# Optimization experiments

Hardware: AMD Instinct MI355X
Metric: run time of the kernel (lower is better)

Reference implementation:

```python
import jax, jax.numpy as jnp
import numpy as np

N_HEADS = 16
MAX_LEN = 1024


def setup_inputs() -> dict:
    key = jax.random.key(0)
    ks = jax.random.split(key, 6)
    B, T, C = 4, 1024, 1024
    scale = 0.02
    return {
        "x": jax.random.normal(ks[0], (B, T, C), dtype=jnp.float32),
        "qkv_w": jax.random.normal(ks[1], (3 * C, C), dtype=jnp.float32) * scale,
        "qkv_b": jax.random.normal(ks[2], (3 * C,), dtype=jnp.float32) * scale,
        "proj_w": jax.random.normal(ks[3], (C, C), dtype=jnp.float32) * scale,
        "proj_b": jax.random.normal(ks[4], (C,), dtype=jnp.float32) * scale,
        "rel_pos_emb": jax.random.normal(ks[5], (2 * MAX_LEN - 1, C), dtype=jnp.float32) * scale,
    }


def reference(x, qkv_w, qkv_b, proj_w, proj_b, rel_pos_emb):
    B, T, C = x.shape
    H = N_HEADS
    D = C // H
    # QKV projection: (B,T,3C) -> (3,B,H,T,D)
    qkv = (x @ qkv_w.T + qkv_b).reshape(B, T, 3, H, D)
    qkv = jnp.transpose(qkv, (2, 0, 3, 1, 4))
    q, k, v = qkv[0], qkv[1], qkv[2]
    # scores: (B,H,T,T)
    att = jnp.einsum("bhtd,bhsd->bhts", q, k) / np.sqrt(D).astype(np.float32)
    # Relative position bias: gather-then-sum == sum-then-gather over head_dim.
    # Pre-reduce table to (2*max_len-1, H) to avoid materializing (T,T,C).
    table = rel_pos_emb.reshape(2 * MAX_LEN - 1, H, D).sum(axis=-1)  # (2L-1, H)
    pos = jnp.arange(T)
    rel_idx = pos[:, None] - pos[None, :] + (MAX_LEN - 1)  # (T,T)
    bias = jnp.transpose(table[rel_idx], (2, 0, 1))  # (H,T,T)
    att = att + bias[None]
    # causal mask: positions j > i masked to -inf
    causal = pos[None, :] > pos[:, None]  # (T,T) True above diagonal
    att = jnp.where(causal[None, None], -jnp.inf, att)
    att = jax.nn.softmax(att, axis=-1)
    out = jnp.einsum("bhts,bhsd->bhtd", att, v)  # (B,H,T,D)
    out = jnp.transpose(out, (0, 2, 1, 3)).reshape(B, T, C)
    return out @ proj_w.T + proj_b
```

## Files before the change

### kernel.cpp

```cpp
#include <hip/hip_runtime.h>
#include <hip/hip_bf16.h>
#include <cstdint>


typedef __bf16 bf16x8 __attribute__((ext_vector_type(8)));
typedef float f32x4 __attribute__((ext_vector_type(4)));

__device__ __forceinline__ float bf2f(unsigned short u) {
    return __uint_as_float(((unsigned)u) << 16);
}
__device__ __forceinline__ unsigned short f2bf(float f) {
    __hip_bfloat16 h = __float2bfloat16(f);
    return *reinterpret_cast<unsigned short*>(&h);
}
__device__ __forceinline__ int4 cvt8(float4 a, float4 b) {
    union { unsigned short s[8]; int4 v; } u;
    u.s[0] = f2bf(a.x); u.s[1] = f2bf(a.y); u.s[2] = f2bf(a.z); u.s[3] = f2bf(a.w);
    u.s[4] = f2bf(b.x); u.s[5] = f2bf(b.y); u.s[6] = f2bf(b.z); u.s[7] = f2bf(b.w);
    return u.v;
}

__device__ __forceinline__ void gload16(const void* g, void* l) {
    __builtin_amdgcn_global_load_lds(
        reinterpret_cast<const __attribute__((address_space(1))) unsigned int*>(
            reinterpret_cast<uintptr_t>(g)),
        reinterpret_cast<__attribute__((address_space(3))) unsigned int*>(
            reinterpret_cast<uintptr_t>(l)),
        16, 0, 0);
}

__global__ __launch_bounds__(256) void cvt3(const float* __restrict__ x,
                                            const float* __restrict__ w1,
                                            const float* __restrict__ w2,
                                            unsigned short* __restrict__ ox,
                                            unsigned short* __restrict__ ow1,
                                            unsigned short* __restrict__ ow2) {
    const int i = blockIdx.x * 256 + threadIdx.x;
    const float* s; unsigned short* d; int li;
    if (i < 524288)      { s = x;  d = ox;  li = i; }
    else if (i < 917504) { s = w1; d = ow1; li = i - 524288; }
    else                 { s = w2; d = ow2; li = i - 917504; }
    const float4 a = *(const float4*)(s + (size_t)li * 8);
    const float4 b = *(const float4*)(s + (size_t)li * 8 + 4);
    *(int4*)(d + (size_t)li * 8) = cvt8(a, b);
}

__global__ __launch_bounds__(256) void table_reduce(const float* __restrict__ rel,
                                                    float* __restrict__ table) {
    const int p = blockIdx.x;
    const int tid = threadIdx.x, lane = tid & 63, wave = tid >> 6;
    const float* r = rel + (size_t)p * 1024;
    float s[4];
#pragma unroll
    for (int k = 0; k < 4; ++k) s[k] = r[tid + 256 * k];
#pragma unroll
    for (int k = 0; k < 4; ++k) {
        float v = s[k];
        for (int o = 32; o; o >>= 1) v += __shfl_xor(v, o, 64);
        if (lane == 0) table[p * 16 + wave + 4 * k] = v;
    }
}

template <int EPI>
__global__ __launch_bounds__(512) void gemm_bt(const unsigned short* __restrict__ A,
                                               const unsigned short* __restrict__ B,
                                               const float* __restrict__ bias,
                                               unsigned short* __restrict__ outb,
                                               float* __restrict__ outf,
                                               int M, int N, int K) {
    __shared__ __attribute__((aligned(16))) unsigned short As[128 * 32];
    __shared__ __attribute__((aligned(16))) unsigned short Bs[128 * 32];
    const int bm = blockIdx.x * 128, bn = blockIdx.y * 128;
    const int tid = threadIdx.x, lane = tid & 63, wave = tid >> 6;
    const int wr = wave & 1, wc = wave >> 1;
    const int quad = lane >> 4, lm = lane & 15;

    const int srow = tid >> 2;
    const int scol = (tid & 3) * 8;
    const unsigned short* Ap = A + (size_t)(bm + srow) * K + scol;
    const unsigned short* Bp = B + (size_t)(bn + srow) * K + scol;
    unsigned short* AsW = &As[tid * 8];
    unsigned short* BsW = &Bs[tid * 8];

    f32x4 acc[4][2];
#pragma unroll
    for (int r = 0; r < 4; ++r)
#pragma unroll
        for (int c = 0; c < 2; ++c) acc[r][c] = (f32x4){0.f, 0.f, 0.f, 0.f};

    for (int kk = 0; kk < K; kk += 32) {
        gload16(Ap + kk, AsW);
        gload16(Bp + kk, BsW);
        __syncthreads();

        bf16x8 af[4], bfr[2];
#pragma unroll
        for (int r = 0; r < 4; ++r)
            af[r] = *(const bf16x8*)(&As[(64 * wr + 16 * r + lm) * 32 + quad * 8]);
#pragma unroll
        for (int c = 0; c < 2; ++c)
            bfr[c] = *(const bf16x8*)(&Bs[(32 * wc + 16 * c + lm) * 32 + quad * 8]);
#pragma unroll
        for (int r = 0; r < 4; ++r)
#pragma unroll
            for (int c = 0; c < 2; ++c)
                acc[r][c] = __builtin_amdgcn_mfma_f32_16x16x32_bf16(af[r], bfr[c], acc[r][c], 0, 0, 0);
        __syncthreads();
    }

#pragma unroll
    for (int r = 0; r < 4; ++r)
#pragma unroll
        for (int c = 0; c < 2; ++c)
#pragma unroll
            for (int i = 0; i < 4; ++i) {
                const int row = bm + 64 * wr + 16 * r + quad * 4 + i;
                const int col = bn + 32 * wc + 16 * c + lm;
                const float v = acc[r][c][i] + bias[col];
                if (EPI == 0) {
                    const int b = row >> 10, t = row & 1023;
                    const int s3 = col >> 10, rem = col & 1023;
                    const int h = rem >> 6, d = rem & 63;
                    const size_t base = (((size_t)s3 * 4 + b) * 16 + h) * 65536;
                    const size_t off = base + (s3 == 2 ? (size_t)d * 1024 + t
                                                       : (size_t)t * 64 + d);
                    outb[off] = f2bf(v);
                } else {
                    outf[(size_t)row * N + col] = v;
                }
            }
}


#define LOADK(DST, KT)                                                        \
    do {                                                                      \
        _Pragma("unroll")                                                     \
        for (int nb = 0; nb < 4; ++nb) {                                      \
            const size_t kr = (size_t)((KT) * 64 + nb * 16 + lm) * 64;        \
            DST[nb * 2]     = *(const bf16x8*)(Kg + kr + quad * 8);           \
            DST[nb * 2 + 1] = *(const bf16x8*)(Kg + kr + 32 + quad * 8);      \
        }                                                                     \
    } while (0)

#define ATTN_TILE(KF, KT)                                                     \
    do {                                                                      \
        const int kt_ = (KT);                                                 \
            \
        bf16x8 vf[8];                                                         \
        _Pragma("unroll")                                                     \
        for (int nb = 0; nb < 4; ++nb) {                                      \
            const size_t vr = (size_t)(nb * 16 + lm) * 1024 + (size_t)kt_ * 64; \
            vf[nb * 2]     = *(const bf16x8*)(Vtg + vr + quad * 8);           \
            vf[nb * 2 + 1] = *(const bf16x8*)(Vtg + vr + 32 + quad * 8);      \
        }                                                                     \
                                \
        f32x4 s[4];                                                           \
        _Pragma("unroll")                                                     \
        for (int nb = 0; nb < 4; ++nb) {                                      \
            s[nb] = (f32x4){0.f, 0.f, 0.f, 0.f};                              \
            s[nb] = __builtin_amdgcn_mfma_f32_16x16x32_bf16(KF[nb * 2], qf0, s[nb], 0, 0, 0); \
            s[nb] = __builtin_amdgcn_mfma_f32_16x16x32_bf16(KF[nb * 2 + 1], qf1, s[nb], 0, 0, 0); \
        }                                                                     \
                    \
        const int jb0 = kt_ * 64 + quad * 4;                                  \
        _Pragma("unroll")                                                     \
        for (int nb = 0; nb < 4; ++nb)                                        \
            _Pragma("unroll")                                                 \
            for (int i = 0; i < 4; ++i) {                                     \
                const int j = jb0 + nb * 16 + i;                              \
                const float v = fmaf(s[nb][i], 0.125f, tb[q - j + 127]);      \
                s[nb][i] = (j <= q) ? v : -1e30f;                             \
            }                                                                 \
              \
        float mx = -1e30f;                                                    \
        _Pragma("unroll")                                                     \
        for (int nb = 0; nb < 4; ++nb)                                        \
            _Pragma("unroll")                                                 \
            for (int i = 0; i < 4; ++i) mx = fmaxf(mx, s[nb][i]);             \
        mx = fmaxf(mx, __shfl_xor(mx, 16, 64));                               \
        mx = fmaxf(mx, __shfl_xor(mx, 32, 64));                               \
        const float mnew = fmaxf(mi, mx);                                     \
        const float alpha = __expf(mi - mnew);                                \
        mi = mnew;                                                            \
        _Pragma("unroll")                                                     \
        for (int nb = 0; nb < 4; ++nb)                                        \
            _Pragma("unroll")                                                 \
            for (int i = 0; i < 4; ++i) s[nb][i] = __expf(s[nb][i] - mnew);   \
        float psum = 0.f;                                                     \
        _Pragma("unroll")                                                     \
        for (int nb = 0; nb < 4; ++nb)                                        \
            psum += (s[nb][0] + s[nb][1]) + (s[nb][2] + s[nb][3]);            \
        psum += __shfl_xor(psum, 16, 64);                                     \
        psum += __shfl_xor(psum, 32, 64);                                     \
        li = li * alpha + psum;                                               \
         \
        _Pragma("unroll")                                                     \
        for (int nb = 0; nb < 4; ++nb) {                                      \
            union { unsigned short u[4]; int2 v; } p4;                        \
            p4.u[0] = f2bf(s[nb][0]);                                         \
            p4.u[1] = f2bf(s[nb][1]);                                         \
            p4.u[2] = f2bf(s[nb][2]);                                         \
            p4.u[3] = f2bf(s[nb][3]);                                         \
            *(int2*)(&Ps[wave][lm][nb * 16 + quad * 4]) = p4.v;               \
        }                                                                     \
                        \
        _Pragma("unroll")                                                     \
        for (int nb = 0; nb < 4; ++nb)                                        \
            _Pragma("unroll")                                                 \
            for (int i = 0; i < 4; ++i) oacc[nb][i] *= alpha;                 \
        const bf16x8 p0 = *(const bf16x8*)(&Ps[wave][lm][quad * 8]);          \
        const bf16x8 p1 = *(const bf16x8*)(&Ps[wave][lm][32 + quad * 8]);     \
                           \
        _Pragma("unroll")                                                     \
        for (int nb = 0; nb < 4; ++nb) {                                      \
            oacc[nb] = __builtin_amdgcn_mfma_f32_16x16x32_bf16(vf[nb * 2], p0, oacc[nb], 0, 0, 0); \
            oacc[nb] = __builtin_amdgcn_mfma_f32_16x16x32_bf16(vf[nb * 2 + 1], p1, oacc[nb], 0, 0, 0); \
        }                                                                     \
    } while (0)

__global__ __launch_bounds__(256) void attn_mfma(const unsigned short* __restrict__ qkvb,
                                                 const float* __restrict__ table,
                                                 unsigned short* __restrict__ y) {
    const int bh = blockIdx.x, b = bh >> 4, h = bh & 15;
    const int level = 15 - blockIdx.y;
    const int tid = threadIdx.x, lane = tid & 63, wave = tid >> 6;
    const int quad = lane >> 4, lm = lane & 15;

    __shared__ __attribute__((aligned(16))) unsigned short Ps[4][16][72];
    __shared__ float tb[1152];

    const unsigned short* Qg  = qkvb + ((size_t)(b)*16 + h) * 65536;
    const unsigned short* Kg  = qkvb + ((size_t)(4 + b)*16 + h) * 65536;
    const unsigned short* Vtg = qkvb + ((size_t)(8 + b)*16 + h) * 65536;

    const int sl = 4 * level + wave;
    const int q = 16 * sl + lm;
    const int ktiles = level + 1;

    const bf16x8 qf0 = *(const bf16x8*)(Qg + (size_t)q * 64 + quad * 8);
    const bf16x8 qf1 = *(const bf16x8*)(Qg + (size_t)q * 64 + 32 + quad * 8);

    const int tbn = 64 * level + 191;
    for (int i = tid; i < tbn; i += 256) tb[i] = table[(896 + i) * 16 + h];
    __syncthreads();

    f32x4 oacc[4];
#pragma unroll
    for (int nb = 0; nb < 4; ++nb) oacc[nb] = (f32x4){0.f, 0.f, 0.f, 0.f};
    float mi = -1e30f, li = 0.f;

    bf16x8 kA[8], kB[8];
    LOADK(kA, 0);
    int kt = 0;
    for (; kt + 2 <= ktiles; kt += 2) {
        LOADK(kB, kt + 1);
        ATTN_TILE(kA, kt);
        if (kt + 2 < ktiles) LOADK(kA, kt + 2);
        ATTN_TILE(kB, kt + 1);
    }
    if (kt < ktiles) ATTN_TILE(kA, kt);

    const float linv = 1.0f / li;
#pragma unroll
    for (int nb = 0; nb < 4; ++nb) {
        union { unsigned short u[4]; int2 v; } o4;
#pragma unroll
        for (int i = 0; i < 4; ++i) o4.u[i] = f2bf(oacc[nb][i] * linv);
        *(int2*)(y + ((size_t)(b * 1024 + q)) * 1024 + h * 64 + nb * 16 + quad * 4) = o4.v;
    }
}

extern "C" void kernel_launch(void* const* d_in, const int* in_sizes, int n_in,
                              void* d_out, int out_size, void* d_ws, size_t ws_size,
                              hipStream_t stream) {
    const float* x      = (const float*)d_in[0];
    const float* qkv_w  = (const float*)d_in[1];
    const float* qkv_b  = (const float*)d_in[2];
    const float* proj_w = (const float*)d_in[3];
    const float* proj_b = (const float*)d_in[4];
    const float* rel    = (const float*)d_in[5];
    float* out = (float*)d_out;

    char* ws = (char*)d_ws;
    unsigned short* xb   = (unsigned short*)(ws + 0);
    unsigned short* qwb  = (unsigned short*)(ws + 8388608);
    unsigned short* pwb  = (unsigned short*)(ws + 14680064);
    float* table         = (float*)(ws + 16777216);
    unsigned short* qkvb = (unsigned short*)(ws + 16908288);
    unsigned short* yb   = (unsigned short*)(ws + 42074112);

    cvt3<<<4096, 256, 0, stream>>>(x, qkv_w, proj_w, xb, qwb, pwb);
    table_reduce<<<2047, 256, 0, stream>>>(rel, table);
    gemm_bt<0><<<dim3(32, 24), 512, 0, stream>>>(xb, qwb, qkv_b, qkvb, nullptr,
                                                 4096, 3072, 1024);
    attn_mfma<<<dim3(64, 16), 256, 0, stream>>>(qkvb, table, yb);
    gemm_bt<1><<<dim3(32, 8), 512, 0, stream>>>(yb, pwb, proj_b, nullptr, out,
                                                4096, 1024, 1024);
}
```

Measured before the change: 221.7 us.

## Split attention softmax state into two independent streams over alternating key tiles

The online-softmax state (running max, sum, output accumulator and P staging buffer) is duplicated so even and odd key tiles update independent chains, which removes the serial dependency between consecutive tiles and lets their MFMA and exp work interleave. The row-sum cross-lane shuffle reduction is deferred from every tile to a single final step. The two partial states are merged at the end by rescaling to a common max. This costs an extra accumulator set in registers and doubles the LDS for P, which may raise register pressure and lower occupancy.

```diff
diff --git a/kernel.cpp b/kernel.cpp
--- a/kernel.cpp
+++ b/kernel.cpp
@@ -142,10 +142,10 @@
         }                                                                     \
     } while (0)
 
-#define ATTN_TILE(KF, KT)                                                     \
+#define ATTN_TILE(KF, KT, MI, LIP, OACC, PSB)                                 \
     do {                                                                      \
         const int kt_ = (KT);                                                 \
-            \
+                     \
         bf16x8 vf[8];                                                         \
         _Pragma("unroll")                                                     \
         for (int nb = 0; nb < 4; ++nb) {                                      \
@@ -171,7 +171,7 @@
                 const float v = fmaf(s[nb][i], 0.125f, tb[q - j + 127]);      \
                 s[nb][i] = (j <= q) ? v : -1e30f;                             \
             }                                                                 \
-              \
+         \
         float mx = -1e30f;                                                    \
         _Pragma("unroll")                                                     \
         for (int nb = 0; nb < 4; ++nb)                                        \
@@ -179,21 +179,19 @@
             for (int i = 0; i < 4; ++i) mx = fmaxf(mx, s[nb][i]);             \
         mx = fmaxf(mx, __shfl_xor(mx, 16, 64));                               \
         mx = fmaxf(mx, __shfl_xor(mx, 32, 64));                               \
-        const float mnew = fmaxf(mi, mx);                                     \
-        const float alpha = __expf(mi - mnew);                                \
-        mi = mnew;                                                            \
+        const float mnew = fmaxf(MI, mx);                                     \
+        const float alpha = __expf(MI - mnew);                                \
+        MI = mnew;                                                            \
         _Pragma("unroll")                                                     \
         for (int nb = 0; nb < 4; ++nb)                                        \
             _Pragma("unroll")                                                 \
             for (int i = 0; i < 4; ++i) s[nb][i] = __expf(s[nb][i] - mnew);   \
-        float psum = 0.f;                                                     \
-        _Pragma("unroll")                                                     \
-        for (int nb = 0; nb < 4; ++nb)                                        \
-            psum += (s[nb][0] + s[nb][1]) + (s[nb][2] + s[nb][3]);            \
-        psum += __shfl_xor(psum, 16, 64);                                     \
-        psum += __shfl_xor(psum, 32, 64);                                     \
-        li = li * alpha + psum;                                               \
-         \
+        float lsum = 0.f;                                                     \
+        _Pragma("unroll")                                                     \
+        for (int nb = 0; nb < 4; ++nb)                                        \
+            lsum += (s[nb][0] + s[nb][1]) + (s[nb][2] + s[nb][3]);            \
+        LIP = LIP * alpha + lsum;             \
+          \
         _Pragma("unroll")                                                     \
         for (int nb = 0; nb < 4; ++nb) {                                      \
             union { unsigned short u[4]; int2 v; } p4;                        \
@@ -201,20 +199,20 @@
             p4.u[1] = f2bf(s[nb][1]);                                         \
             p4.u[2] = f2bf(s[nb][2]);                                         \
             p4.u[3] = f2bf(s[nb][3]);                                         \
-            *(int2*)(&Ps[wave][lm][nb * 16 + quad * 4]) = p4.v;               \
+            *(int2*)(&PSB[wave][lm][nb * 16 + quad * 4]) = p4.v;              \
         }                                                                     \
                         \
         _Pragma("unroll")                                                     \
         for (int nb = 0; nb < 4; ++nb)                                        \
             _Pragma("unroll")                                                 \
-            for (int i = 0; i < 4; ++i) oacc[nb][i] *= alpha;                 \
-        const bf16x8 p0 = *(const bf16x8*)(&Ps[wave][lm][quad * 8]);          \
-        const bf16x8 p1 = *(const bf16x8*)(&Ps[wave][lm][32 + quad * 8]);     \
+            for (int i = 0; i < 4; ++i) OACC[nb][i] *= alpha;                 \
+        const bf16x8 p0 = *(const bf16x8*)(&PSB[wave][lm][quad * 8]);         \
+        const bf16x8 p1 = *(const bf16x8*)(&PSB[wave][lm][32 + quad * 8]);    \
                            \
         _Pragma("unroll")                                                     \
         for (int nb = 0; nb < 4; ++nb) {                                      \
-            oacc[nb] = __builtin_amdgcn_mfma_f32_16x16x32_bf16(vf[nb * 2], p0, oacc[nb], 0, 0, 0); \
-            oacc[nb] = __builtin_amdgcn_mfma_f32_16x16x32_bf16(vf[nb * 2 + 1], p1, oacc[nb], 0, 0, 0); \
+            OACC[nb] = __builtin_amdgcn_mfma_f32_16x16x32_bf16(vf[nb * 2], p0, OACC[nb], 0, 0, 0); \
+            OACC[nb] = __builtin_amdgcn_mfma_f32_16x16x32_bf16(vf[nb * 2 + 1], p1, OACC[nb], 0, 0, 0); \
         }                                                                     \
     } while (0)
 
@@ -226,7 +224,7 @@
     const int tid = threadIdx.x, lane = tid & 63, wave = tid >> 6;
     const int quad = lane >> 4, lm = lane & 15;
 
-    __shared__ __attribute__((aligned(16))) unsigned short Ps[4][16][72];
+    __shared__ __attribute__((aligned(16))) unsigned short Ps[2][4][16][72];
     __shared__ float tb[1152];
 
     const unsigned short* Qg  = qkvb + ((size_t)(b)*16 + h) * 65536;
@@ -244,28 +242,39 @@
     for (int i = tid; i < tbn; i += 256) tb[i] = table[(896 + i) * 16 + h];
     __syncthreads();
 
-    f32x4 oacc[4];
-#pragma unroll
-    for (int nb = 0; nb < 4; ++nb) oacc[nb] = (f32x4){0.f, 0.f, 0.f, 0.f};
-    float mi = -1e30f, li = 0.f;
+    f32x4 oa0[4], oa1[4];
+#pragma unroll
+    for (int nb = 0; nb < 4; ++nb) {
+        oa0[nb] = (f32x4){0.f, 0.f, 0.f, 0.f};
+        oa1[nb] = (f32x4){0.f, 0.f, 0.f, 0.f};
+    }
+    float mi0 = -1e30f, li0 = 0.f;
+    float mi1 = -1e30f, li1 = 0.f;
 
     bf16x8 kA[8], kB[8];
     LOADK(kA, 0);
     int kt = 0;
     for (; kt + 2 <= ktiles; kt += 2) {
         LOADK(kB, kt + 1);
-        ATTN_TILE(kA, kt);
+        ATTN_TILE(kA, kt, mi0, li0, oa0, Ps[0]);
         if (kt + 2 < ktiles) LOADK(kA, kt + 2);
-        ATTN_TILE(kB, kt + 1);
-    }
-    if (kt < ktiles) ATTN_TILE(kA, kt);
-
-    const float linv = 1.0f / li;
+        ATTN_TILE(kB, kt + 1, mi1, li1, oa1, Ps[1]);
+    }
+    if (kt < ktiles) ATTN_TILE(kA, kt, mi0, li0, oa0, Ps[0]);
+
+    const float mstar = fmaxf(mi0, mi1);
+    const float w0 = __expf(mi0 - mstar), w1 = __expf(mi1 - mstar);
+    float lip = li0 * w0 + li1 * w1;
+    lip += __shfl_xor(lip, 16, 64);
+    lip += __shfl_xor(lip, 32, 64);
+    const float linv = 1.0f / lip;
+
 #pragma unroll
     for (int nb = 0; nb < 4; ++nb) {
         union { unsigned short u[4]; int2 v; } o4;
 #pragma unroll
-        for (int i = 0; i < 4; ++i) o4.u[i] = f2bf(oacc[nb][i] * linv);
+        for (int i = 0; i < 4; ++i)
+            o4.u[i] = f2bf((oa0[nb][i] * w0 + oa1[nb][i] * w1) * linv);
         *(int2*)(y + ((size_t)(b * 1024 + q)) * 1024 + h * 64 + nb * 16 + quad * 4) = o4.v;
     }
 }
```

Result: no change. 224.0 us (+1.1%).

## Switch attention to 32x32x16 MFMA with register-shuffled P and finer causal tiles

Applied to the files above, without the earlier changes.

Rewrites the attention kernel to use 32x32x16 bf16 MFMA. Each wave now handles 32 query rows with 32-key tiles, using two waves per block instead of four. The softmax probabilities are repacked into B operands through cross-lane shuffles instead of an LDS round-trip. The causal mask is applied only on diagonal tiles, and the per-wave tile count follows the causal boundary at 32-key granularity. Halving the block size lowers per-block parallelism and may change occupancy and latency hiding.

```diff
diff --git a/kernel.cpp b/kernel.cpp
--- a/kernel.cpp
+++ b/kernel.cpp
@@ -5,6 +5,7 @@
 
 typedef __bf16 bf16x8 __attribute__((ext_vector_type(8)));
 typedef float f32x4 __attribute__((ext_vector_type(4)));
+typedef float f32x16 __attribute__((ext_vector_type(16)));
 
 __device__ __forceinline__ float bf2f(unsigned short u) {
     return __uint_as_float(((unsigned)u) << 16);
@@ -12,6 +13,9 @@
 __device__ __forceinline__ unsigned short f2bf(float f) {
     __hip_bfloat16 h = __float2bfloat16(f);
     return *reinterpret_cast<unsigned short*>(&h);
+}
+__device__ __forceinline__ unsigned pk2(float a, float b) {
+    return (unsigned)f2bf(a) | ((unsigned)f2bf(b) << 16);
 }
 __device__ __forceinline__ int4 cvt8(float4 a, float4 b) {
     union { unsigned short s[8]; int4 v; } u;
@@ -131,142 +135,142 @@
             }
 }
 
-
 #define LOADK(DST, KT)                                                        \
     do {                                                                      \
-        _Pragma("unroll")                                                     \
-        for (int nb = 0; nb < 4; ++nb) {                                      \
-            const size_t kr = (size_t)((KT) * 64 + nb * 16 + lm) * 64;        \
-            DST[nb * 2]     = *(const bf16x8*)(Kg + kr + quad * 8);           \
-            DST[nb * 2 + 1] = *(const bf16x8*)(Kg + kr + 32 + quad * 8);      \
-        }                                                                     \
+        const unsigned short* kr_ = Kg + (size_t)((KT) * 32 + l5) * 64 + hi8; \
+        DST[0] = *(const bf16x8*)(kr_);                                       \
+        DST[1] = *(const bf16x8*)(kr_ + 16);                                  \
+        DST[2] = *(const bf16x8*)(kr_ + 32);                                  \
+        DST[3] = *(const bf16x8*)(kr_ + 48);                                  \
     } while (0)
 
 #define ATTN_TILE(KF, KT)                                                     \
     do {                                                                      \
         const int kt_ = (KT);                                                 \
-            \
-        bf16x8 vf[8];                                                         \
-        _Pragma("unroll")                                                     \
-        for (int nb = 0; nb < 4; ++nb) {                                      \
-            const size_t vr = (size_t)(nb * 16 + lm) * 1024 + (size_t)kt_ * 64; \
-            vf[nb * 2]     = *(const bf16x8*)(Vtg + vr + quad * 8);           \
-            vf[nb * 2 + 1] = *(const bf16x8*)(Vtg + vr + 32 + quad * 8);      \
+        const int jb = kt_ * 32;                                              \
+         \
+        const unsigned short* vb_ = Vtg + (size_t)l5 * 1024 + jb + hi8;       \
+        const bf16x8 vf00 = *(const bf16x8*)(vb_);                            \
+        const bf16x8 vf01 = *(const bf16x8*)(vb_ + 16);                       \
+        const bf16x8 vf10 = *(const bf16x8*)(vb_ + 32768);                    \
+        const bf16x8 vf11 = *(const bf16x8*)(vb_ + 32768 + 16);               \
+                                    \
+        f32x16 s = {0.f};                                                     \
+        _Pragma("unroll")                                                     \
+        for (int t = 0; t < 4; ++t)                                           \
+            s = __builtin_amdgcn_mfma_f32_32x32x16_bf16(KF[t], qf[t], s, 0, 0, 0); \
+         \
+        float p[16];                                                          \
+        _Pragma("unroll")                                                     \
+        for (int reg = 0; reg < 16; ++reg) {                                  \
+            const int j = jb + (reg & 3) + 8 * (reg >> 2) + 4 * hi;           \
+            p[reg] = fmaf(s[reg], 0.125f, tb[q - j + 127]);                   \
         }                                                                     \
-                                \
-        f32x4 s[4];                                                           \
-        _Pragma("unroll")                                                     \
-        for (int nb = 0; nb < 4; ++nb) {                                      \
-            s[nb] = (f32x4){0.f, 0.f, 0.f, 0.f};                              \
-            s[nb] = __builtin_amdgcn_mfma_f32_16x16x32_bf16(KF[nb * 2], qf0, s[nb], 0, 0, 0); \
-            s[nb] = __builtin_amdgcn_mfma_f32_16x16x32_bf16(KF[nb * 2 + 1], qf1, s[nb], 0, 0, 0); \
+        if (jb + 31 > qbase) {         \
+            _Pragma("unroll")                                                 \
+            for (int reg = 0; reg < 16; ++reg) {                              \
+                const int j = jb + (reg & 3) + 8 * (reg >> 2) + 4 * hi;       \
+                p[reg] = (j <= q) ? p[reg] : -1e30f;                          \
+            }                                                                 \
         }                                                                     \
-                    \
-        const int jb0 = kt_ * 64 + quad * 4;                                  \
-        _Pragma("unroll")                                                     \
-        for (int nb = 0; nb < 4; ++nb)                                        \
-            _Pragma("unroll")                                                 \
-            for (int i = 0; i < 4; ++i) {                                     \
-                const int j = jb0 + nb * 16 + i;                              \
-                const float v = fmaf(s[nb][i], 0.125f, tb[q - j + 127]);      \
-                s[nb][i] = (j <= q) ? v : -1e30f;                             \
-            }                                                                 \
-              \
-        float mx = -1e30f;                                                    \
-        _Pragma("unroll")                                                     \
-        for (int nb = 0; nb < 4; ++nb)                                        \
-            _Pragma("unroll")                                                 \
-            for (int i = 0; i < 4; ++i) mx = fmaxf(mx, s[nb][i]);             \
-        mx = fmaxf(mx, __shfl_xor(mx, 16, 64));                               \
+                                  \
+        float mx = p[0];                                                      \
+        _Pragma("unroll")                                                     \
+        for (int reg = 1; reg < 16; ++reg) mx = fmaxf(mx, p[reg]);            \
         mx = fmaxf(mx, __shfl_xor(mx, 32, 64));                               \
         const float mnew = fmaxf(mi, mx);                                     \
         const float alpha = __expf(mi - mnew);                                \
         mi = mnew;                                                            \
-        _Pragma("unroll")                                                     \
-        for (int nb = 0; nb < 4; ++nb)                                        \
-            _Pragma("unroll")                                                 \
-            for (int i = 0; i < 4; ++i) s[nb][i] = __expf(s[nb][i] - mnew);   \
-        float psum = 0.f;                                                     \
-        _Pragma("unroll")                                                     \
-        for (int nb = 0; nb < 4; ++nb)                                        \
-            psum += (s[nb][0] + s[nb][1]) + (s[nb][2] + s[nb][3]);            \
-        psum += __shfl_xor(psum, 16, 64);                                     \
-        psum += __shfl_xor(psum, 32, 64);                                     \
-        li = li * alpha + psum;                                               \
-         \
-        _Pragma("unroll")                                                     \
-        for (int nb = 0; nb < 4; ++nb) {                                      \
-            union { unsigned short u[4]; int2 v; } p4;                        \
-            p4.u[0] = f2bf(s[nb][0]);                                         \
-            p4.u[1] = f2bf(s[nb][1]);                                         \
-            p4.u[2] = f2bf(s[nb][2]);                                         \
-            p4.u[3] = f2bf(s[nb][3]);                                         \
-            *(int2*)(&Ps[wave][lm][nb * 16 + quad * 4]) = p4.v;               \
+        float lsum = 0.f;                                                     \
+        _Pragma("unroll")                                                     \
+        for (int reg = 0; reg < 16; ++reg) {                                  \
+            p[reg] = __expf(p[reg] - mnew);                                   \
+            lsum += p[reg];                                                   \
+        }                                                                     \
+        li = li * alpha + lsum;     \
+                \
+        const unsigned P0 = pk2(p[0], p[1]),   P1 = pk2(p[2], p[3]);          \
+        const unsigned P2 = pk2(p[4], p[5]),   P3 = pk2(p[6], p[7]);          \
+        const unsigned P4 = pk2(p[8], p[9]),   P5 = pk2(p[10], p[11]);        \
+        const unsigned P6 = pk2(p[12], p[13]), P7 = pk2(p[14], p[15]);        \
+        const unsigned R0 = __shfl_xor(hi ? P0 : P2, 32, 64);                 \
+        const unsigned R1 = __shfl_xor(hi ? P1 : P3, 32, 64);                 \
+        const unsigned R2 = __shfl_xor(hi ? P4 : P6, 32, 64);                 \
+        const unsigned R3 = __shfl_xor(hi ? P5 : P7, 32, 64);                 \
+        union { unsigned w[4]; bf16x8 v; } bq0, bq1;                          \
+        bq0.w[0] = hi ? R0 : P0;  bq0.w[1] = hi ? R1 : P1;                    \
+        bq0.w[2] = hi ? P2 : R0;  bq0.w[3] = hi ? P3 : R1;                    \
+        bq1.w[0] = hi ? R2 : P4;  bq1.w[1] = hi ? R3 : P5;                    \
+        bq1.w[2] = hi ? P6 : R2;  bq1.w[3] = hi ? P7 : R3;                    \
+                                 \
+        _Pragma("unroll")                                                     \
+        for (int reg = 0; reg < 16; ++reg) {                                  \
+            oa0[reg] *= alpha;                                                \
+            oa1[reg] *= alpha;                                                \
         }                                                                     \
                         \
-        _Pragma("unroll")                                                     \
-        for (int nb = 0; nb < 4; ++nb)                                        \
-            _Pragma("unroll")                                                 \
-            for (int i = 0; i < 4; ++i) oacc[nb][i] *= alpha;                 \
-        const bf16x8 p0 = *(const bf16x8*)(&Ps[wave][lm][quad * 8]);          \
-        const bf16x8 p1 = *(const bf16x8*)(&Ps[wave][lm][32 + quad * 8]);     \
-                           \
-        _Pragma("unroll")                                                     \
-        for (int nb = 0; nb < 4; ++nb) {                                      \
-            oacc[nb] = __builtin_amdgcn_mfma_f32_16x16x32_bf16(vf[nb * 2], p0, oacc[nb], 0, 0, 0); \
-            oacc[nb] = __builtin_amdgcn_mfma_f32_16x16x32_bf16(vf[nb * 2 + 1], p1, oacc[nb], 0, 0, 0); \
-        }                                                                     \
+        oa0 = __builtin_amdgcn_mfma_f32_32x32x16_bf16(vf00, bq0.v, oa0, 0, 0, 0); \
+        oa0 = __builtin_amdgcn_mfma_f32_32x32x16_bf16(vf01, bq1.v, oa0, 0, 0, 0); \
+        oa1 = __builtin_amdgcn_mfma_f32_32x32x16_bf16(vf10, bq0.v, oa1, 0, 0, 0); \
+        oa1 = __builtin_amdgcn_mfma_f32_32x32x16_bf16(vf11, bq1.v, oa1, 0, 0, 0); \
     } while (0)
 
-__global__ __launch_bounds__(256) void attn_mfma(const unsigned short* __restrict__ qkvb,
+__global__ __launch_bounds__(128) void attn_mfma(const unsigned short* __restrict__ qkvb,
                                                  const float* __restrict__ table,
                                                  unsigned short* __restrict__ y) {
     const int bh = blockIdx.x, b = bh >> 4, h = bh & 15;
     const int level = 15 - blockIdx.y;
     const int tid = threadIdx.x, lane = tid & 63, wave = tid >> 6;
-    const int quad = lane >> 4, lm = lane & 15;
-
-    __shared__ __attribute__((aligned(16))) unsigned short Ps[4][16][72];
+    const int l5 = lane & 31, hi = lane >> 5, hi8 = hi * 8;
+
     __shared__ float tb[1152];
 
     const unsigned short* Qg  = qkvb + ((size_t)(b)*16 + h) * 65536;
     const unsigned short* Kg  = qkvb + ((size_t)(4 + b)*16 + h) * 65536;
     const unsigned short* Vtg = qkvb + ((size_t)(8 + b)*16 + h) * 65536;
 
-    const int sl = 4 * level + wave;
-    const int q = 16 * sl + lm;
-    const int ktiles = level + 1;
-
-    const bf16x8 qf0 = *(const bf16x8*)(Qg + (size_t)q * 64 + quad * 8);
-    const bf16x8 qf1 = *(const bf16x8*)(Qg + (size_t)q * 64 + 32 + quad * 8);
+    const int qbase = 64 * level + 32 * wave;
+    const int q = qbase + l5;
+    const int nt = 2 * level + wave + 1;
+
+    bf16x8 qf[4];
+    {
+        const unsigned short* qr = Qg + (size_t)q * 64 + hi8;
+#pragma unroll
+        for (int t = 0; t < 4; ++t) qf[t] = *(const bf16x8*)(qr + t * 16);
+    }
 
     const int tbn = 64 * level + 191;
-    for (int i = tid; i < tbn; i += 256) tb[i] = table[(896 + i) * 16 + h];
+    for (int i = tid; i < tbn; i += 128) tb[i] = table[(896 + i) * 16 + h];
     __syncthreads();
 
-    f32x4 oacc[4];
-#pragma unroll
-    for (int nb = 0; nb < 4; ++nb) oacc[nb] = (f32x4){0.f, 0.f, 0.f, 0.f};
+    f32x16 oa0 = {0.f}, oa1 = {0.f};
     float mi = -1e30f, li = 0.f;
 
-    bf16x8 kA[8], kB[8];
+    bf16x8 kA[4], kB[4];
     LOADK(kA, 0);
     int kt = 0;
-    for (; kt + 2 <= ktiles; kt += 2) {
+    for (; kt + 2 <= nt; kt += 2) {
         LOADK(kB, kt + 1);
         ATTN_TILE(kA, kt);
-        if (kt + 2 < ktiles) LOADK(kA, kt + 2);
+        if (kt + 2 < nt) LOADK(kA, kt + 2);
         ATTN_TILE(kB, kt + 1);
     }
-    if (kt < ktiles) ATTN_TILE(kA, kt);
-
+    if (kt < nt) ATTN_TILE(kA, kt);
+
+    li += __shfl_xor(li, 32, 64);
     const float linv = 1.0f / li;
-#pragma unroll
-    for (int nb = 0; nb < 4; ++nb) {
-        union { unsigned short u[4]; int2 v; } o4;
-#pragma unroll
-        for (int i = 0; i < 4; ++i) o4.u[i] = f2bf(oacc[nb][i] * linv);
-        *(int2*)(y + ((size_t)(b * 1024 + q)) * 1024 + h * 64 + nb * 16 + quad * 4) = o4.v;
+    unsigned short* yq = y + ((size_t)(b * 1024 + q)) * 1024 + h * 64;
+#pragma unroll
+    for (int g = 0; g < 4; ++g) {
+        union { unsigned short u[4]; int2 v; } o4a, o4b;
+#pragma unroll
+        for (int i = 0; i < 4; ++i) {
+            o4a.u[i] = f2bf(oa0[4 * g + i] * linv);
+            o4b.u[i] = f2bf(oa1[4 * g + i] * linv);
+        }
+        *(int2*)(yq + 8 * g + 4 * hi) = o4a.v;
+        *(int2*)(yq + 32 + 8 * g + 4 * hi) = o4b.v;
     }
 }
 
@@ -293,7 +297,7 @@
     table_reduce<<<2047, 256, 0, stream>>>(rel, table);
     gemm_bt<0><<<dim3(32, 24), 512, 0, stream>>>(xb, qwb, qkv_b, qkvb, nullptr,
                                                  4096, 3072, 1024);
-    attn_mfma<<<dim3(64, 16), 256, 0, stream>>>(qkvb, table, yb);
+    attn_mfma<<<dim3(64, 16), 128, 0, stream>>>(qkvb, table, yb);
     gemm_bt<1><<<dim3(32, 8), 512, 0, stream>>>(yb, pwb, proj_b, nullptr, out,
                                                 4096, 1024, 1024);
 }
```

Result: faster. 197.7 us (-10.8%).
